# Performance work log

Measured on AMD Instinct MI355X. Metric: run time of the kernel, lower is better.

Reference implementation:

```python
import jax, jax.numpy as jnp
import numpy as np

B, H, SQ, SKV, D = 2, 16, 2048, 2048, 128
EMBED_DIM = H * D  # 2048; temperature init = embedding_dim // num_heads = 128


def setup_inputs() -> dict:
    key = jax.random.key(0)
    kq, kk, kv = jax.random.split(key, 3)
    query = jax.random.normal(kq, (B, H, SQ, D), dtype=jnp.float32)
    k = jax.random.normal(kk, (B, H, SKV, D), dtype=jnp.float32)
    value = jax.random.normal(kv, (B, H, SKV, D), dtype=jnp.float32)
    # learnable per-head temperature, initialized to embedding_dim // num_heads
    temperature = jnp.ones((1, H, 1, 1), dtype=jnp.float32) * (EMBED_DIM // H)
    return {"query": query, "key": k, "value": value, "temperature": temperature}


def reference(query, key, value, temperature):
    # qk = Q @ K^T  -> [B, H, Sq, Skv]
    qk = jnp.einsum("bhqd,bhkd->bhqk", query, key)
    scaled_qk = qk * (1.0 / temperature)  # per-head learnable inverse scale
    attn = jax.nn.softmax(scaled_qk, axis=-1)
    # dropout is identity in eval / p=0
    out = jnp.einsum("bhqk,bhkd->bhqd", attn, value)
    return out
```

## Files before the change

### kernel.cpp

```cpp
#include <hip/hip_runtime.h>
#include <cstdint>
#include <cstddef>

#define BB 2
#define HH 16
#define SQ 2048
#define SKV 2048
#define DD 128

#define QT 256
#define KT 64
#define NT (SKV / KT)
#define KSTR 136
#define VSTR 72
#define KBUF (64 * KSTR)
#define VBUF (128 * VSTR)

typedef __attribute__((ext_vector_type(8))) short short8;
typedef __attribute__((ext_vector_type(16))) float floatx16;

#define LDS_BARRIER() asm volatile("s_waitcnt lgkmcnt(0)\n\ts_barrier" ::: "memory")

__device__ __forceinline__ unsigned short f2bf(float f) {
    union { float f; unsigned u; } x;
    x.f = f;
    unsigned r = x.u + 0x7fffu + ((x.u >> 16) & 1u);
    return (unsigned short)(r >> 16);
}

__device__ __forceinline__ unsigned cvt_pk_bf16(float a, float b) {
    unsigned r;
    asm("v_cvt_pk_bf16_f32 %0, %1, %2" : "=v"(r) : "v"(a), "v"(b));
    return r;
}

__global__ __launch_bounds__(256) void conv_k_kernel(const float* __restrict__ K,
                                                     unsigned short* __restrict__ Kb)
{
    size_t idx = ((size_t)blockIdx.x * 256 + threadIdx.x) * 8;
    float4 a = *(const float4*)(K + idx);
    float4 b = *(const float4*)(K + idx + 4);
    short8 o;
    o[0] = (short)f2bf(a.x); o[1] = (short)f2bf(a.y);
    o[2] = (short)f2bf(a.z); o[3] = (short)f2bf(a.w);
    o[4] = (short)f2bf(b.x); o[5] = (short)f2bf(b.y);
    o[6] = (short)f2bf(b.z); o[7] = (short)f2bf(b.w);
    *(short8*)(Kb + idx) = o;
}

__global__ __launch_bounds__(256) void trans_v_kernel(const float* __restrict__ V,
                                                      unsigned short* __restrict__ Vtb)
{
    __shared__ __align__(16) unsigned short lds[DD * VSTR];
    const int tid = threadIdx.x;
    const int kvt = blockIdx.x;
    const int bh  = blockIdx.y;

    const float* Vp = V + ((size_t)bh * SKV + (size_t)kvt * KT) * DD;
#pragma unroll
    for (int it = 0; it < 8; ++it) {
        int f4   = it * 256 + tid;
        int row  = f4 >> 5;
        int prow = (row & ~12) | ((row & 4) << 1) | ((row & 8) >> 1);
        int col4 = (f4 & 31) << 2;
        float4 v = *(const float4*)(Vp + (size_t)row * DD + col4);
        lds[(col4 + 0) * VSTR + prow] = f2bf(v.x);
        lds[(col4 + 1) * VSTR + prow] = f2bf(v.y);
        lds[(col4 + 2) * VSTR + prow] = f2bf(v.z);
        lds[(col4 + 3) * VSTR + prow] = f2bf(v.w);
    }
    __syncthreads();
#pragma unroll
    for (int it = 0; it < 4; ++it) {
        int idx = it * 256 + tid;
        int d   = idx >> 3;
        int c8  = (idx & 7) << 3;
        short8 s = *(const short8*)&lds[d * VSTR + c8];
        *(short8*)(Vtb + ((size_t)bh * DD + d) * SKV + (size_t)kvt * KT + c8) = s;
    }
}

__global__ __launch_bounds__(512, 2) void fattn_kernel(
    const float* __restrict__ Q, const unsigned short* __restrict__ Kb,
    const unsigned short* __restrict__ Vtb, const float* __restrict__ T,
    float* __restrict__ O)
{
    __shared__ __align__(16) unsigned short lds_k[2][KBUF];
    __shared__ __align__(16) unsigned short lds_v[2][VBUF];

    const int tid  = threadIdx.x;
    const int wave = tid >> 6;
    const int lane = tid & 63;
    const int l31  = lane & 31;
    const int hi   = lane >> 5;

    const int wg    = blockIdx.x;
    const int bh    = (wg & 7) * 4 + ((wg >> 3) & 3);
    const int qtile = wg >> 5;
    const int h     = bh & (HH - 1);

    const float scale = 1.44269504088896f / T[h];

    const float*          Qp  = Q   + (size_t)bh * SQ * DD;
    const unsigned short* Kp  = Kb  + (size_t)bh * SKV * DD;
    const unsigned short* Vtp = Vtb + (size_t)bh * DD * SKV;
    float*                Op  = O   + (size_t)bh * SQ * DD;

    short8 qf[8];
    {
        const int qrow = qtile * QT + wave * 32 + l31;
#pragma unroll
        for (int ks = 0; ks < 8; ++ks) {
            const float* p = Qp + (size_t)qrow * DD + ks * 16 + hi * 8;
            float4 a = *(const float4*)(p);
            float4 b = *(const float4*)(p + 4);
            short8 q;
            q[0] = (short)f2bf(a.x * scale); q[1] = (short)f2bf(a.y * scale);
            q[2] = (short)f2bf(a.z * scale); q[3] = (short)f2bf(a.w * scale);
            q[4] = (short)f2bf(b.x * scale); q[5] = (short)f2bf(b.y * scale);
            q[6] = (short)f2bf(b.z * scale); q[7] = (short)f2bf(b.w * scale);
            qf[ks] = q;
        }
    }

    floatx16 oacc[4];
#pragma unroll
    for (int dt = 0; dt < 4; ++dt)
#pragma unroll
        for (int r = 0; r < 16; ++r) oacc[dt][r] = 0.f;
    float psum = 0.f;

    const int kcr = tid >> 4;
    const int kcc = (tid & 15) << 3;
    const int vcr = tid >> 3;
    const int vcc = (tid & 7) << 3;

    short8 kp0, kp1, vp0, vp1;

#define LOADT(t) do { \
        const unsigned short* kt_ = Kp + (size_t)(t) * KT * DD; \
        const unsigned short* vt_ = Vtp + (size_t)(t) * KT; \
        kp0 = *(const short8*)(kt_ + (size_t)kcr * DD + kcc); \
        kp1 = *(const short8*)(kt_ + (size_t)(kcr + 32) * DD + kcc); \
        vp0 = *(const short8*)(vt_ + (size_t)vcr * SKV + vcc); \
        vp1 = *(const short8*)(vt_ + (size_t)(vcr + 64) * SKV + vcc); \
    } while (0)

#define STAGET(buf) do { \
        *(short8*)&lds_k[buf][kcr * KSTR + kcc] = kp0; \
        *(short8*)&lds_k[buf][(kcr + 32) * KSTR + kcc] = kp1; \
        *(short8*)&lds_v[buf][vcr * VSTR + vcc] = vp0; \
        *(short8*)&lds_v[buf][(vcr + 64) * VSTR + vcc] = vp1; \
    } while (0)

    LOADT(0);
    STAGET(0);
    LOADT(1);
    LDS_BARRIER();

    for (int t = 0; t < NT; ++t) {
        const int cur = t & 1;
        const unsigned short* lk = lds_k[cur];
        const unsigned short* lv = lds_v[cur];

        floatx16 s0, s1;
#pragma unroll
        for (int r = 0; r < 16; ++r) { s0[r] = 0.f; s1[r] = 0.f; }
        __builtin_amdgcn_s_setprio(1);
#pragma unroll
        for (int ks = 0; ks < 8; ++ks) {
            short8 kf0 = *(const short8*)&lk[(l31     ) * KSTR + ks * 16 + hi * 8];
            short8 kf1 = *(const short8*)&lk[(l31 + 32) * KSTR + ks * 16 + hi * 8];
            s0 = __builtin_amdgcn_mfma_f32_32x32x16_bf16(kf0, qf[ks], s0, 0, 0, 0);
            s1 = __builtin_amdgcn_mfma_f32_32x32x16_bf16(kf1, qf[ks], s1, 0, 0, 0);
        }
        __builtin_amdgcn_s_setprio(0);

        unsigned pk0[8], pk1[8];
#pragma unroll
        for (int i = 0; i < 8; ++i) {
            float e0 = __builtin_amdgcn_exp2f(s0[2 * i]);
            float e1 = __builtin_amdgcn_exp2f(s0[2 * i + 1]);
            float e2 = __builtin_amdgcn_exp2f(s1[2 * i]);
            float e3 = __builtin_amdgcn_exp2f(s1[2 * i + 1]);
            psum += (e0 + e1) + (e2 + e3);
            pk0[i] = cvt_pk_bf16(e0, e1);
            pk1[i] = cvt_pk_bf16(e2, e3);
        }
        union { unsigned u[4]; short8 s8; } ap[2][2];
#pragma unroll
        for (int w = 0; w < 4; ++w) {
            ap[0][0].u[w] = pk0[w];
            ap[0][1].u[w] = pk0[w + 4];
            ap[1][0].u[w] = pk1[w];
            ap[1][1].u[w] = pk1[w + 4];
        }

        if (t + 1 < NT) STAGET(cur ^ 1);

        __builtin_amdgcn_s_setprio(1);
#pragma unroll
        for (int kvt = 0; kvt < 2; ++kvt)
#pragma unroll
            for (int s = 0; s < 2; ++s) {
                const int cb = kvt * 32 + s * 16 + hi * 8;
#pragma unroll
                for (int dt = 0; dt < 4; ++dt) {
                    short8 vf = *(const short8*)&lv[(dt * 32 + l31) * VSTR + cb];
                    oacc[dt] = __builtin_amdgcn_mfma_f32_32x32x16_bf16(
                        ap[kvt][s].s8, vf, oacc[dt], 0, 0, 0);
                }
            }
        __builtin_amdgcn_s_setprio(0);

        if (t + 2 < NT) LOADT(t + 2);

        LDS_BARRIER();
    }

    float tot = psum + __shfl_xor(psum, 32, 64);
    float inv = 1.0f / tot;
    float ivr[16];
#pragma unroll
    for (int r = 0; r < 16; ++r) {
        const int ql = (r & 3) + 8 * (r >> 2) + 4 * hi;
        ivr[r] = __shfl(inv, ql, 64);
    }
    const int qbase = qtile * QT + wave * 32;
#pragma unroll
    for (int dt = 0; dt < 4; ++dt)
#pragma unroll
        for (int r = 0; r < 16; ++r) {
            const int ql = (r & 3) + 8 * (r >> 2) + 4 * hi;
            Op[(size_t)(qbase + ql) * DD + dt * 32 + l31] = oacc[dt][r] * ivr[r];
        }
#undef LOADT
#undef STAGET
}

extern "C" void kernel_launch(void* const* d_in, const int* in_sizes, int n_in,
                              void* d_out, int out_size, void* d_ws, size_t ws_size,
                              hipStream_t stream) {
    const float* Q = (const float*)d_in[0];
    const float* K = (const float*)d_in[1];
    const float* V = (const float*)d_in[2];
    const float* T = (const float*)d_in[3];
    float* O = (float*)d_out;

    unsigned short* Kb  = (unsigned short*)d_ws;
    unsigned short* Vtb = Kb + (size_t)BB * HH * SKV * DD;

    const size_t nK = (size_t)BB * HH * SKV * DD;
    conv_k_kernel<<<dim3(nK / (256 * 8)), 256, 0, stream>>>(K, Kb);
    trans_v_kernel<<<dim3(SKV / KT, BB * HH), 256, 0, stream>>>(V, Vtb);

    fattn_kernel<<<dim3((SQ / QT) * BB * HH), 512, 0, stream>>>(Q, Kb, Vtb, T, O);
}
```

Before: 194.4 us.

## Use direct global-to-LDS loads with pre-swizzled K/V tile images

```diff
diff --git a/kernel.cpp b/kernel.cpp
--- a/kernel.cpp
+++ b/kernel.cpp
@@ -8,18 +8,17 @@
 #define SKV 2048
 #define DD 128
 
-#define QT 256
+#define QT 128
 #define KT 64
 #define NT (SKV / KT)
-#define KSTR 136
-#define VSTR 72
-#define KBUF (64 * KSTR)
-#define VBUF (128 * VSTR)
+
+#define KIMG_T 8192
+#define VIMG_T 8192
 
 typedef __attribute__((ext_vector_type(8))) short short8;
 typedef __attribute__((ext_vector_type(16))) float floatx16;
 
-#define LDS_BARRIER() asm volatile("s_waitcnt lgkmcnt(0)\n\ts_barrier" ::: "memory")
+#define TILE_BARRIER() asm volatile("s_waitcnt vmcnt(0) lgkmcnt(0)\n\ts_barrier" ::: "memory")
 
 __device__ __forceinline__ unsigned short f2bf(float f) {
     union { float f; unsigned u; } x;
@@ -34,65 +33,85 @@
     return r;
 }
 
-__global__ __launch_bounds__(256) void conv_k_kernel(const float* __restrict__ K,
-                                                     unsigned short* __restrict__ Kb)
+__device__ __forceinline__ void gload16(const void* g, void* l) {
+    __builtin_amdgcn_global_load_lds(
+        (const __attribute__((address_space(1))) unsigned int*)g,
+        (__attribute__((address_space(3))) unsigned int*)l, 16, 0, 0);
+}
+
+__device__ __forceinline__ int swap23(int r) {
+    return (r & ~12) | ((r & 4) << 1) | ((r & 8) >> 1);
+}
+
+__global__ __launch_bounds__(256) void prep_kernel(const float* __restrict__ K,
+                                                   const float* __restrict__ V,
+                                                   unsigned short* __restrict__ Kimg,
+                                                   unsigned short* __restrict__ Vimg)
 {
-    size_t idx = ((size_t)blockIdx.x * 256 + threadIdx.x) * 8;
-    float4 a = *(const float4*)(K + idx);
-    float4 b = *(const float4*)(K + idx + 4);
-    short8 o;
-    o[0] = (short)f2bf(a.x); o[1] = (short)f2bf(a.y);
-    o[2] = (short)f2bf(a.z); o[3] = (short)f2bf(a.w);
-    o[4] = (short)f2bf(b.x); o[5] = (short)f2bf(b.y);
-    o[6] = (short)f2bf(b.z); o[7] = (short)f2bf(b.w);
-    *(short8*)(Kb + idx) = o;
-}
-
-__global__ __launch_bounds__(256) void trans_v_kernel(const float* __restrict__ V,
-                                                      unsigned short* __restrict__ Vtb)
-{
-    __shared__ __align__(16) unsigned short lds[DD * VSTR];
+    __shared__ __align__(16) unsigned short lds[DD * 72];
     const int tid = threadIdx.x;
     const int kvt = blockIdx.x;
     const int bh  = blockIdx.y;
 
+    const float* Kp = K + ((size_t)bh * SKV + (size_t)kvt * KT) * DD;
+    unsigned short* Kout = Kimg + ((size_t)bh * NT + kvt) * KIMG_T;
+#pragma unroll
+    for (int i = 0; i < 4; ++i) {
+        int c   = i * 256 + tid;
+        int row = c >> 4;
+        int s   = c & 15;
+        const float* p = Kp + (size_t)row * DD + s * 8;
+        float4 a = *(const float4*)(p);
+        float4 b = *(const float4*)(p + 4);
+        short8 o;
+        o[0] = (short)f2bf(a.x); o[1] = (short)f2bf(a.y);
+        o[2] = (short)f2bf(a.z); o[3] = (short)f2bf(a.w);
+        o[4] = (short)f2bf(b.x); o[5] = (short)f2bf(b.y);
+        o[6] = (short)f2bf(b.z); o[7] = (short)f2bf(b.w);
+        *(short8*)&Kout[row * 128 + ((s ^ (row & 7)) * 8)] = o;
+    }
+
     const float* Vp = V + ((size_t)bh * SKV + (size_t)kvt * KT) * DD;
 #pragma unroll
-    for (int it = 0; it < 8; ++it) {
-        int f4   = it * 256 + tid;
-        int row  = f4 >> 5;
-        int prow = (row & ~12) | ((row & 4) << 1) | ((row & 8) >> 1);
-        int col4 = (f4 & 31) << 2;
-        float4 v = *(const float4*)(Vp + (size_t)row * DD + col4);
-        lds[(col4 + 0) * VSTR + prow] = f2bf(v.x);
-        lds[(col4 + 1) * VSTR + prow] = f2bf(v.y);
-        lds[(col4 + 2) * VSTR + prow] = f2bf(v.z);
-        lds[(col4 + 3) * VSTR + prow] = f2bf(v.w);
+    for (int it = 0; it < 4; ++it) {
+        int idx  = it * 256 + tid;
+        int rp   = idx >> 5;
+        int col4 = (idx & 31) << 2;
+        int r0 = rp * 2;
+        float4 va = *(const float4*)(Vp + (size_t)r0 * DD + col4);
+        float4 vb = *(const float4*)(Vp + (size_t)(r0 + 1) * DD + col4);
+        int p0 = swap23(r0);
+        *(unsigned*)&lds[(col4 + 0) * 72 + p0] = cvt_pk_bf16(va.x, vb.x);
+        *(unsigned*)&lds[(col4 + 1) * 72 + p0] = cvt_pk_bf16(va.y, vb.y);
+        *(unsigned*)&lds[(col4 + 2) * 72 + p0] = cvt_pk_bf16(va.z, vb.z);
+        *(unsigned*)&lds[(col4 + 3) * 72 + p0] = cvt_pk_bf16(va.w, vb.w);
     }
     __syncthreads();
-#pragma unroll
-    for (int it = 0; it < 4; ++it) {
-        int idx = it * 256 + tid;
-        int d   = idx >> 3;
-        int c8  = (idx & 7) << 3;
-        short8 s = *(const short8*)&lds[d * VSTR + c8];
-        *(short8*)(Vtb + ((size_t)bh * DD + d) * SKV + (size_t)kvt * KT + c8) = s;
-    }
-}
-
-__global__ __launch_bounds__(512, 2) void fattn_kernel(
-    const float* __restrict__ Q, const unsigned short* __restrict__ Kb,
-    const unsigned short* __restrict__ Vtb, const float* __restrict__ T,
+    unsigned short* Vout = Vimg + ((size_t)bh * NT + kvt) * VIMG_T;
+#pragma unroll
+    for (int i = 0; i < 4; ++i) {
+        int c = i * 256 + tid;
+        int d = c >> 3;
+        int s = c & 7;
+        short8 x = *(const short8*)&lds[d * 72 + s * 8];
+        *(short8*)&Vout[d * 64 + ((s ^ (d & 7)) * 8)] = x;
+    }
+}
+
+__global__ __launch_bounds__(256, 2) void fattn_kernel(
+    const float* __restrict__ Q, const unsigned short* __restrict__ Kimg,
+    const unsigned short* __restrict__ Vimg, const float* __restrict__ T,
     float* __restrict__ O)
 {
-    __shared__ __align__(16) unsigned short lds_k[2][KBUF];
-    __shared__ __align__(16) unsigned short lds_v[2][VBUF];
-
-    const int tid  = threadIdx.x;
-    const int wave = tid >> 6;
-    const int lane = tid & 63;
-    const int l31  = lane & 31;
-    const int hi   = lane >> 5;
+    __shared__ __align__(16) unsigned short lds_k[2][KIMG_T];
+    __shared__ __align__(16) unsigned short lds_v[2][VIMG_T];
+
+    const int tid   = threadIdx.x;
+    const int wbase = tid & ~63;
+    const int lane  = tid & 63;
+    const int l31   = lane & 31;
+    const int hi    = lane >> 5;
+    const int xw    = l31 & 7;
 
     const int wg    = blockIdx.x;
     const int bh    = (wg & 7) * 4 + ((wg >> 3) & 3);
@@ -101,14 +120,26 @@
 
     const float scale = 1.44269504088896f / T[h];
 
-    const float*          Qp  = Q   + (size_t)bh * SQ * DD;
-    const unsigned short* Kp  = Kb  + (size_t)bh * SKV * DD;
-    const unsigned short* Vtp = Vtb + (size_t)bh * DD * SKV;
-    float*                Op  = O   + (size_t)bh * SQ * DD;
+    const float*          Qp = Q    + (size_t)bh * SQ * DD;
+    const unsigned short* Kp = Kimg + (size_t)bh * NT * KIMG_T;
+    const unsigned short* Vp = Vimg + (size_t)bh * NT * VIMG_T;
+    float*                Op = O    + (size_t)bh * SQ * DD;
+
+#define ISSUE(t, buf) do { \
+        const unsigned short* kg_ = Kp + (size_t)(t) * KIMG_T; \
+        const unsigned short* vg_ = Vp + (size_t)(t) * VIMG_T; \
+        _Pragma("unroll") \
+        for (int i_ = 0; i_ < 4; ++i_) { \
+            gload16(kg_ + (size_t)(i_ * 256 + tid) * 8, &lds_k[buf][(i_ * 256 + wbase) * 8]); \
+            gload16(vg_ + (size_t)(i_ * 256 + tid) * 8, &lds_v[buf][(i_ * 256 + wbase) * 8]); \
+        } \
+    } while (0)
+
+    ISSUE(0, 0);
 
     short8 qf[8];
     {
-        const int qrow = qtile * QT + wave * 32 + l31;
+        const int qrow = qtile * QT + (tid >> 6) * 32 + l31;
 #pragma unroll
         for (int ks = 0; ks < 8; ++ks) {
             const float* p = Qp + (size_t)qrow * DD + ks * 16 + hi * 8;
@@ -130,92 +161,82 @@
         for (int r = 0; r < 16; ++r) oacc[dt][r] = 0.f;
     float psum = 0.f;
 
-    const int kcr = tid >> 4;
-    const int kcc = (tid & 15) << 3;
-    const int vcr = tid >> 3;
-    const int vcc = (tid & 7) << 3;
-
-    short8 kp0, kp1, vp0, vp1;
-
-#define LOADT(t) do { \
-        const unsigned short* kt_ = Kp + (size_t)(t) * KT * DD; \
-        const unsigned short* vt_ = Vtp + (size_t)(t) * KT; \
-        kp0 = *(const short8*)(kt_ + (size_t)kcr * DD + kcc); \
-        kp1 = *(const short8*)(kt_ + (size_t)(kcr + 32) * DD + kcc); \
-        vp0 = *(const short8*)(vt_ + (size_t)vcr * SKV + vcc); \
-        vp1 = *(const short8*)(vt_ + (size_t)(vcr + 64) * SKV + vcc); \
-    } while (0)
-
-#define STAGET(buf) do { \
-        *(short8*)&lds_k[buf][kcr * KSTR + kcc] = kp0; \
-        *(short8*)&lds_k[buf][(kcr + 32) * KSTR + kcc] = kp1; \
-        *(short8*)&lds_v[buf][vcr * VSTR + vcc] = vp0; \
-        *(short8*)&lds_v[buf][(vcr + 64) * VSTR + vcc] = vp1; \
-    } while (0)
-
-    LOADT(0);
-    STAGET(0);
-    LOADT(1);
-    LDS_BARRIER();
+    asm volatile("s_waitcnt vmcnt(0)\n\ts_barrier" ::: "memory");
 
     for (int t = 0; t < NT; ++t) {
         const int cur = t & 1;
         const unsigned short* lk = lds_k[cur];
         const unsigned short* lv = lds_v[cur];
 
+        if (t + 1 < NT) ISSUE(t + 1, cur ^ 1);
+
         floatx16 s0, s1;
 #pragma unroll
         for (int r = 0; r < 16; ++r) { s0[r] = 0.f; s1[r] = 0.f; }
         __builtin_amdgcn_s_setprio(1);
 #pragma unroll
         for (int ks = 0; ks < 8; ++ks) {
-            short8 kf0 = *(const short8*)&lk[(l31     ) * KSTR + ks * 16 + hi * 8];
-            short8 kf1 = *(const short8*)&lk[(l31 + 32) * KSTR + ks * 16 + hi * 8];
+            const int ko = ((2 * ks + hi) ^ xw) * 8;
+            short8 kf0 = *(const short8*)&lk[(l31     ) * 128 + ko];
+            short8 kf1 = *(const short8*)&lk[(l31 + 32) * 128 + ko];
             s0 = __builtin_amdgcn_mfma_f32_32x32x16_bf16(kf0, qf[ks], s0, 0, 0, 0);
             s1 = __builtin_amdgcn_mfma_f32_32x32x16_bf16(kf1, qf[ks], s1, 0, 0, 0);
         }
         __builtin_amdgcn_s_setprio(0);
 
-        unsigned pk0[8], pk1[8];
-#pragma unroll
-        for (int i = 0; i < 8; ++i) {
-            float e0 = __builtin_amdgcn_exp2f(s0[2 * i]);
-            float e1 = __builtin_amdgcn_exp2f(s0[2 * i + 1]);
-            float e2 = __builtin_amdgcn_exp2f(s1[2 * i]);
-            float e3 = __builtin_amdgcn_exp2f(s1[2 * i + 1]);
-            psum += (e0 + e1) + (e2 + e3);
-            pk0[i] = cvt_pk_bf16(e0, e1);
-            pk1[i] = cvt_pk_bf16(e2, e3);
-        }
         union { unsigned u[4]; short8 s8; } ap[2][2];
-#pragma unroll
-        for (int w = 0; w < 4; ++w) {
-            ap[0][0].u[w] = pk0[w];
-            ap[0][1].u[w] = pk0[w + 4];
-            ap[1][0].u[w] = pk1[w];
-            ap[1][1].u[w] = pk1[w + 4];
-        }
-
-        if (t + 1 < NT) STAGET(cur ^ 1);
+
+        {
+            unsigned pk[8];
+#pragma unroll
+            for (int i = 0; i < 8; ++i) {
+                float e0 = __builtin_amdgcn_exp2f(s0[2 * i]);
+                float e1 = __builtin_amdgcn_exp2f(s0[2 * i + 1]);
+                psum += e0 + e1;
+                pk[i] = cvt_pk_bf16(e0, e1);
+            }
+#pragma unroll
+            for (int w = 0; w < 4; ++w) { ap[0][0].u[w] = pk[w]; ap[0][1].u[w] = pk[w + 4]; }
+        }
 
         __builtin_amdgcn_s_setprio(1);
 #pragma unroll
-        for (int kvt = 0; kvt < 2; ++kvt)
-#pragma unroll
-            for (int s = 0; s < 2; ++s) {
-                const int cb = kvt * 32 + s * 16 + hi * 8;
-#pragma unroll
-                for (int dt = 0; dt < 4; ++dt) {
-                    short8 vf = *(const short8*)&lv[(dt * 32 + l31) * VSTR + cb];
-                    oacc[dt] = __builtin_amdgcn_mfma_f32_32x32x16_bf16(
-                        ap[kvt][s].s8, vf, oacc[dt], 0, 0, 0);
-                }
-            }
+        for (int s2 = 0; s2 < 2; ++s2) {
+            const int vo = ((2 * s2 + hi) ^ xw) * 8;
+#pragma unroll
+            for (int dt = 0; dt < 4; ++dt) {
+                short8 vf = *(const short8*)&lv[(dt * 32 + l31) * 64 + vo];
+                oacc[dt] = __builtin_amdgcn_mfma_f32_32x32x16_bf16(ap[0][s2].s8, vf, oacc[dt], 0, 0, 0);
+            }
+        }
         __builtin_amdgcn_s_setprio(0);
 
-        if (t + 2 < NT) LOADT(t + 2);
-
-        LDS_BARRIER();
+        {
+            unsigned pk[8];
+#pragma unroll
+            for (int i = 0; i < 8; ++i) {
+                float e0 = __builtin_amdgcn_exp2f(s1[2 * i]);
+                float e1 = __builtin_amdgcn_exp2f(s1[2 * i + 1]);
+                psum += e0 + e1;
+                pk[i] = cvt_pk_bf16(e0, e1);
+            }
+#pragma unroll
+            for (int w = 0; w < 4; ++w) { ap[1][0].u[w] = pk[w]; ap[1][1].u[w] = pk[w + 4]; }
+        }
+
+        __builtin_amdgcn_s_setprio(1);
+#pragma unroll
+        for (int s2 = 0; s2 < 2; ++s2) {
+            const int vo = ((4 + 2 * s2 + hi) ^ xw) * 8;
+#pragma unroll
+            for (int dt = 0; dt < 4; ++dt) {
+                short8 vf = *(const short8*)&lv[(dt * 32 + l31) * 64 + vo];
+                oacc[dt] = __builtin_amdgcn_mfma_f32_32x32x16_bf16(ap[1][s2].s8, vf, oacc[dt], 0, 0, 0);
+            }
+        }
+        __builtin_amdgcn_s_setprio(0);
+
+        TILE_BARRIER();
     }
 
     float tot = psum + __shfl_xor(psum, 32, 64);
@@ -226,7 +247,7 @@
         const int ql = (r & 3) + 8 * (r >> 2) + 4 * hi;
         ivr[r] = __shfl(inv, ql, 64);
     }
-    const int qbase = qtile * QT + wave * 32;
+    const int qbase = qtile * QT + (tid >> 6) * 32;
 #pragma unroll
     for (int dt = 0; dt < 4; ++dt)
 #pragma unroll
@@ -234,8 +255,7 @@
             const int ql = (r & 3) + 8 * (r >> 2) + 4 * hi;
             Op[(size_t)(qbase + ql) * DD + dt * 32 + l31] = oacc[dt][r] * ivr[r];
         }
-#undef LOADT
-#undef STAGET
+#undef ISSUE
 }
 
 extern "C" void kernel_launch(void* const* d_in, const int* in_sizes, int n_in,
@@ -247,12 +267,9 @@
     const float* T = (const float*)d_in[3];
     float* O = (float*)d_out;
 
-    unsigned short* Kb  = (unsigned short*)d_ws;
-    unsigned short* Vtb = Kb + (size_t)BB * HH * SKV * DD;
-
-    const size_t nK = (size_t)BB * HH * SKV * DD;
-    conv_k_kernel<<<dim3(nK / (256 * 8)), 256, 0, stream>>>(K, Kb);
-    trans_v_kernel<<<dim3(SKV / KT, BB * HH), 256, 0, stream>>>(V, Vtb);
-
-    fattn_kernel<<<dim3((SQ / QT) * BB * HH), 512, 0, stream>>>(Q, Kb, Vtb, T, O);
-}
+    unsigned short* Kimg = (unsigned short*)d_ws;
+    unsigned short* Vimg = Kimg + (size_t)BB * HH * NT * KIMG_T;
+
+    prep_kernel<<<dim3(NT, BB * HH), 256, 0, stream>>>(K, V, Kimg, Vimg);
+    fattn_kernel<<<dim3((SQ / QT) * BB * HH), 256, 0, stream>>>(Q, Kimg, Vimg, T, O);
+}
```

Result: slower. 207.0 us (+6.5%).
